# Optimization experiments

Hardware: AMD Instinct MI355X
Metric: run time of the kernel (lower is better)

The kernel has to match this reference:

```python
import jax, jax.numpy as jnp
import numpy as np

EPS_D = 1e-8   # clamp_min on knn distances
EPS_BN = 1e-5  # BatchNorm eps
K = 3


def _cdist(a, b):
    # a: (B,M,3), b: (B,N,3) -> (B,M,N) euclidean distances
    a2 = jnp.sum(a * a, axis=-1)[:, :, None]
    b2 = jnp.sum(b * b, axis=-1)[:, None, :]
    ab = jnp.einsum('bmd,bnd->bmn', a, b)
    return jnp.sqrt(jnp.maximum(a2 + b2 - 2.0 * ab, 0.0))


def _bn_relu(x, gamma, beta):
    # x: (B,C,N); BatchNorm1d training-mode math (biased batch stats) + ReLU
    mean = jnp.mean(x, axis=(0, 2), keepdims=True)
    var = jnp.mean((x - mean) ** 2, axis=(0, 2), keepdims=True)
    xn = (x - mean) * jax.lax.rsqrt(var + EPS_BN)
    return jax.nn.relu(xn * gamma[None, :, None] + beta[None, :, None])


def setup_inputs() -> dict:
    key = jax.random.key(0)
    ks = jax.random.split(key, 6)
    B, N1, N2, C1, C2 = 8, 8192, 2048, 128, 256
    xyz1 = jax.random.normal(ks[0], (B, N1, 3), dtype=jnp.float32)
    xyz2 = jax.random.normal(ks[1], (B, N2, 3), dtype=jnp.float32)
    feats1 = jax.random.normal(ks[2], (B, C1, N1), dtype=jnp.float32)
    feats2 = jax.random.normal(ks[3], (B, C2, N2), dtype=jnp.float32)
    in_ch = C2 + C1  # 384
    W1 = jax.random.normal(ks[4], (256, in_ch), dtype=jnp.float32) * 0.05
    b1 = jnp.zeros((256,), jnp.float32)
    g1 = jnp.ones((256,), jnp.float32)
    be1 = jnp.zeros((256,), jnp.float32)
    W2 = jax.random.normal(ks[5], (128, 256), dtype=jnp.float32) * 0.05
    b2 = jnp.zeros((128,), jnp.float32)
    g2 = jnp.ones((128,), jnp.float32)
    be2 = jnp.zeros((128,), jnp.float32)
    return {"xyz1": xyz1, "xyz2": xyz2, "feats1": feats1, "feats2": feats2,
            "W1": W1, "b1": b1, "g1": g1, "be1": be1,
            "W2": W2, "b2": b2, "g2": g2, "be2": be2}


def reference(xyz1, xyz2, feats1, feats2, W1, b1, g1, be1, W2, b2, g2, be2):
    # --- KNN interpolation ---
    d = _cdist(xyz1, xyz2)                       # (B,N1,N2)
    _, idx = jax.lax.top_k(-d, K)                # smallest-K indices (B,N1,K)
    knn_d = jnp.take_along_axis(d, idx, axis=2)  # (B,N1,K)
    w = 1.0 / jnp.maximum(knn_d, EPS_D)
    w = w / jnp.sum(w, axis=-1, keepdims=True)
    f2p = jnp.swapaxes(feats2, 1, 2)             # (B,N2,C2)
    neigh = jax.vmap(lambda f, i: f[i])(f2p, idx)  # (B,N1,K,C2)
    out = jnp.einsum('bmk,bmkc->bmc', w, neigh)  # (B,N1,C2)
    out = jnp.swapaxes(out, 1, 2)                # (B,C2,N1)
    out = jnp.concatenate([out, feats1], axis=1) # (B,C2+C1,N1)
    # --- Conv1d(1)-BN-ReLU MLP ---
    h = jnp.einsum('oc,bcn->bon', W1, out) + b1[None, :, None]
    h = _bn_relu(h, g1, be1)
    h = jnp.einsum('oc,bcn->bon', W2, h) + b2[None, :, None]
    h = _bn_relu(h, g2, be2)
    return h
```

## Files before the change

kernel.cpp:

```cpp
#include <hip/hip_runtime.h>

typedef __attribute__((ext_vector_type(8))) short short8;
typedef __attribute__((ext_vector_type(4))) float f32x4;

#define GLDS(gp, lp) __builtin_amdgcn_global_load_lds( \
    (const __attribute__((address_space(1))) void*)(gp), \
    (__attribute__((address_space(3))) void*)(lp), 16, 0, 0)

__device__ __forceinline__ unsigned short f2bf(float f){
    unsigned u = __float_as_uint(f);
    unsigned r = (u + 0x7fffu + ((u >> 16) & 1u)) >> 16;
    return (unsigned short)r;
}
__device__ __forceinline__ float bf2f(unsigned short s){
    return __uint_as_float(((unsigned)s) << 16);
}

__global__ __launch_bounds__(256) void cast_w_kernel(const float* __restrict__ W1, const float* __restrict__ W2,
                                                     unsigned short* __restrict__ W1c, unsigned short* __restrict__ W2c){
    int i = blockIdx.x * 256 + threadIdx.x;
    if (i < 98304) W1c[i] = f2bf(W1[i]);
    if (i < 32768) W2c[i] = f2bf(W2[i]);
}

__global__ void zero_stats_kernel(float* __restrict__ s){
    int i = blockIdx.x * 256 + threadIdx.x;
    if (i < 768) s[i] = 0.f;
}

__global__ __launch_bounds__(256) void knn_kernel(const float* __restrict__ xyz1, const float* __restrict__ xyz2,
                                                  int* __restrict__ oi, float* __restrict__ ow){
    __shared__ float sx[2048], sy[2048], sz[2048];
    __shared__ float sd[64][25];
    __shared__ int   si[64][25];
    int blk = blockIdx.x;
    int b  = blk >> 7;
    int n0 = (blk & 127) << 6;
    const float* p2 = xyz2 + (size_t)b * 2048 * 3;
    for (int j = threadIdx.x; j < 2048; j += 256){
        sx[j] = p2[j*3+0]; sy[j] = p2[j*3+1]; sz[j] = p2[j*3+2];
    }
    __syncthreads();
    int pp = threadIdx.x & 31, sub = threadIdx.x >> 5;
    int pA = n0 + pp, pB = pA + 32;
    const float* qa = xyz1 + ((size_t)b * 8192 + pA) * 3;
    float ax = qa[0], ay = qa[1], az = qa[2];
    float bx = qa[96], by = qa[97], bz = qa[98];
    float A0 = 1e30f, A1 = 1e30f, A2 = 1e30f; int Ai0 = 0, Ai1 = 0, Ai2 = 0;
    float B0 = 1e30f, B1 = 1e30f, B2 = 1e30f; int Bi0 = 0, Bi1 = 0, Bi2 = 0;
    int jb = sub << 8;
#pragma unroll 2
    for (int i = 0; i < 256; i += 4){
        f32x4 cx = *(const f32x4*)&sx[jb + i];
        f32x4 cy = *(const f32x4*)&sy[jb + i];
        f32x4 cz = *(const f32x4*)&sz[jb + i];
#pragma unroll
        for (int u = 0; u < 4; ++u){
            int j = jb + i + u;
            float dxA = ax - cx[u], dyA = ay - cy[u], dzA = az - cz[u];
            float dA = fmaf(dxA, dxA, fmaf(dyA, dyA, dzA * dzA));
            float dxB = bx - cx[u], dyB = by - cy[u], dzB = bz - cz[u];
            float dB = fmaf(dxB, dxB, fmaf(dyB, dyB, dzB * dzB));
            if (dA < A2){
                if (dA < A1){
                    A2 = A1; Ai2 = Ai1;
                    if (dA < A0){ A1 = A0; Ai1 = Ai0; A0 = dA; Ai0 = j; }
                    else        { A1 = dA; Ai1 = j; }
                } else { A2 = dA; Ai2 = j; }
            }
            if (dB < B2){
                if (dB < B1){
                    B2 = B1; Bi2 = Bi1;
                    if (dB < B0){ B1 = B0; Bi1 = Bi0; B0 = dB; Bi0 = j; }
                    else        { B1 = dB; Bi1 = j; }
                } else { B2 = dB; Bi2 = j; }
            }
        }
    }
    int c = sub * 3;
    sd[pp][c] = A0; sd[pp][c+1] = A1; sd[pp][c+2] = A2;
    si[pp][c] = Ai0; si[pp][c+1] = Ai1; si[pp][c+2] = Ai2;
    sd[pp+32][c] = B0; sd[pp+32][c+1] = B1; sd[pp+32][c+2] = B2;
    si[pp+32][c] = Bi0; si[pp+32][c+1] = Bi1; si[pp+32][c+2] = Bi2;
    __syncthreads();
    if (threadIdx.x < 64){
        int lp = threadIdx.x;
        float d0 = 1e30f, d1 = 1e30f, d2 = 1e30f;
        int i0 = 0, i1 = 0, i2 = 0;
#pragma unroll
        for (int k = 0; k < 24; ++k){
            float d = sd[lp][k]; int j = si[lp][k];
            if (d < d2){
                if (d < d1){
                    d2 = d1; i2 = i1;
                    if (d < d0){ d1 = d0; i1 = i0; d0 = d; i0 = j; }
                    else        { d1 = d;  i1 = j; }
                } else { d2 = d; i2 = j; }
            }
        }
        float w0 = 1.f / fmaxf(sqrtf(d0), 1e-8f);
        float w1 = 1.f / fmaxf(sqrtf(d1), 1e-8f);
        float w2 = 1.f / fmaxf(sqrtf(d2), 1e-8f);
        float inv = 1.f / (w0 + w1 + w2);
        int n = n0 + lp;
        size_t pbase = ((size_t)b * 8192 + n) * 3;
        ow[pbase + 0] = w0 * inv; ow[pbase + 1] = w1 * inv; ow[pbase + 2] = w2 * inv;
        oi[pbase + 0] = i0;       oi[pbase + 1] = i1;       oi[pbase + 2] = i2;
    }
}

__global__ __launch_bounds__(256) void transpose_f2_kernel(const float* __restrict__ f2, unsigned short* __restrict__ f2t){
    __shared__ float tile[32][33];
    int b = blockIdx.z, c0 = blockIdx.y * 32, n0 = blockIdx.x * 32;
    int tx = threadIdx.x, ty = threadIdx.y;
    for (int i = 0; i < 32; i += 8)
        tile[ty + i][tx] = f2[((size_t)b * 256 + c0 + ty + i) * 2048 + n0 + tx];
    __syncthreads();
    for (int i = 0; i < 32; i += 8)
        f2t[((size_t)b * 2048 + n0 + ty + i) * 256 + c0 + tx] = f2bf(tile[tx][ty + i]);
}

__global__ __launch_bounds__(128) void interp_kernel(const int* __restrict__ ki, const float* __restrict__ kw,
                                                     const unsigned short* __restrict__ f2t, unsigned short* __restrict__ X){
    int p = blockIdx.x;
    int b = p >> 13;
    const int*   ip = ki + (size_t)p * 3;
    const float* wp = kw + (size_t)p * 3;
    int i0 = ip[0], i1 = ip[1], i2 = ip[2];
    float w0 = wp[0], w1 = wp[1], w2 = wp[2];
    int t = threadIdx.x;
    const unsigned* f0 = (const unsigned*)(f2t + ((size_t)b * 2048 + i0) * 256);
    const unsigned* f1 = (const unsigned*)(f2t + ((size_t)b * 2048 + i1) * 256);
    const unsigned* f2 = (const unsigned*)(f2t + ((size_t)b * 2048 + i2) * 256);
    unsigned a = f0[t], c = f1[t], d = f2[t];
    float r0 = w0 * bf2f((unsigned short)(a & 0xffff)) + w1 * bf2f((unsigned short)(c & 0xffff)) + w2 * bf2f((unsigned short)(d & 0xffff));
    float r1 = w0 * bf2f((unsigned short)(a >> 16))   + w1 * bf2f((unsigned short)(c >> 16))   + w2 * bf2f((unsigned short)(d >> 16));
    ((unsigned*)(X + (size_t)p * 384))[t] = (unsigned)f2bf(r0) | ((unsigned)f2bf(r1) << 16);
}

__global__ __launch_bounds__(256) void transpose_f1_kernel(const float* __restrict__ f1, unsigned short* __restrict__ X){
    __shared__ float tile[32][33];
    int b = blockIdx.z, c0 = blockIdx.y * 32, n0 = blockIdx.x * 32;
    int tx = threadIdx.x, ty = threadIdx.y;
    for (int i = 0; i < 32; i += 8)
        tile[ty + i][tx] = f1[((size_t)b * 128 + c0 + ty + i) * 8192 + n0 + tx];
    __syncthreads();
    for (int i = 0; i < 32; i += 8)
        X[((size_t)b * 8192 + n0 + ty + i) * 384 + 256 + c0 + tx] = f2bf(tile[tx][ty + i]);
}

template<int KT, bool OBF>
__global__ __launch_bounds__(256) void gemm_bt(const unsigned short* __restrict__ A, const unsigned short* __restrict__ Bt,
                                               const float* __restrict__ bias, void* __restrict__ Cout,
                                               float* __restrict__ gsum, float* __restrict__ gsq, int Ncols){
    __shared__ unsigned short As[128 * 32];
    __shared__ unsigned short Bs[128 * 32];
    __shared__ float sLs[128], sLq[128];
    int tid = threadIdx.x;
    if (tid < 128){ sLs[tid] = 0.f; sLq[tid] = 0.f; }
    int m0 = blockIdx.x * 128;
    int n0 = blockIdx.y * 128;
    int lane = tid & 63, wid = tid >> 6;
    int m_w = (wid >> 1) * 64, n_w = (wid & 1) * 64;
    f32x4 acc[4][4] = {};

    int srow = tid >> 2, schunk = tid & 3;
    const char* Ab = (const char*)A + ((size_t)(m0 + srow) * KT + schunk * 8) * 2;
    const char* Bb = (const char*)Bt + ((size_t)(n0 + srow) * KT + schunk * 8) * 2;
    char* Asl = (char*)As + tid * 16;
    char* Bsl = (char*)Bs + tid * 16;
    const size_t rstep = (size_t)64 * KT * 2;

    int lr = lane & 15, lq = lane >> 4;
    for (int kt = 0; kt < KT / 32; ++kt){
        size_t koff = (size_t)kt * 64;
        GLDS(Ab + koff, Asl);
        GLDS(Ab + koff + rstep, Asl + 4096);
        GLDS(Bb + koff, Bsl);
        GLDS(Bb + koff + rstep, Bsl + 4096);
        __syncthreads();
        short8 af[4], bfr[4];
#pragma unroll
        for (int mf = 0; mf < 4; ++mf)
            af[mf] = *(const short8*)(As + (m_w + mf * 16 + lr) * 32 + lq * 8);
#pragma unroll
        for (int nf = 0; nf < 4; ++nf)
            bfr[nf] = *(const short8*)(Bs + (n_w + nf * 16 + lr) * 32 + lq * 8);
#pragma unroll
        for (int mf = 0; mf < 4; ++mf)
#pragma unroll
            for (int nf = 0; nf < 4; ++nf)
                acc[mf][nf] = __builtin_amdgcn_mfma_f32_16x16x32_bf16(af[mf], bfr[nf], acc[mf][nf], 0, 0, 0);
        __syncthreads();
    }

#pragma unroll
    for (int nf = 0; nf < 4; ++nf){
        int cl = n_w + nf * 16 + lr;
        int gc = n0 + cl;
        float bv = bias[gc];
        float ps = 0.f, pq = 0.f;
#pragma unroll
        for (int mf = 0; mf < 4; ++mf){
            int grow = m0 + m_w + mf * 16 + lq * 4;
#pragma unroll
            for (int r = 0; r < 4; ++r){
                float v = acc[mf][nf][r] + bv;
                size_t off = (size_t)(grow + r) * Ncols + gc;
                if (OBF) ((unsigned short*)Cout)[off] = f2bf(v);
                else     ((float*)Cout)[off] = v;
                ps += v; pq += v * v;
            }
        }
        ps += __shfl_xor(ps, 16); ps += __shfl_xor(ps, 32);
        pq += __shfl_xor(pq, 16); pq += __shfl_xor(pq, 32);
        if (lq == 0){ atomicAdd(&sLs[cl], ps); atomicAdd(&sLq[cl], pq); }
    }
    __syncthreads();
    if (tid < 128){
        atomicAdd(&gsum[n0 + tid], sLs[tid]);
        atomicAdd(&gsq[n0 + tid],  sLq[tid]);
    }
}

__global__ __launch_bounds__(256) void bn_relu_bf16(unsigned short* __restrict__ h, const float* __restrict__ gsum,
                                                    const float* __restrict__ gsq, const float* __restrict__ gamma,
                                                    const float* __restrict__ beta){
    const float inv = 1.0f / 65536.0f;
    size_t total2 = (size_t)65536 * 128;
    unsigned* hp = (unsigned*)h;
    for (size_t i = (size_t)blockIdx.x * blockDim.x + threadIdx.x; i < total2; i += (size_t)gridDim.x * blockDim.x){
        int c0 = (int)((i * 2) & 255);
        unsigned v = hp[i];
        float x0 = bf2f((unsigned short)(v & 0xffff));
        float x1 = bf2f((unsigned short)(v >> 16));
        float m0 = gsum[c0] * inv,     m1 = gsum[c0 + 1] * inv;
        float va0 = gsq[c0] * inv - m0 * m0, va1 = gsq[c0 + 1] * inv - m1 * m1;
        float rs0 = rsqrtf(va0 + 1e-5f), rs1 = rsqrtf(va1 + 1e-5f);
        float y0 = fmaxf((x0 - m0) * rs0 * gamma[c0] + beta[c0], 0.f);
        float y1 = fmaxf((x1 - m1) * rs1 * gamma[c0 + 1] + beta[c0 + 1], 0.f);
        hp[i] = (unsigned)f2bf(y0) | ((unsigned)f2bf(y1) << 16);
    }
}

__global__ __launch_bounds__(256) void bn2_transpose_kernel(const float* __restrict__ h2, const float* __restrict__ gsum,
                                                            const float* __restrict__ gsq, const float* __restrict__ g2,
                                                            const float* __restrict__ be2, float* __restrict__ out){
    __shared__ float tile[32][33];
    const float inv = 1.0f / 65536.0f;
    int b = blockIdx.z, o0 = blockIdx.y * 32, n0 = blockIdx.x * 32;
    int tx = threadIdx.x, ty = threadIdx.y;
    for (int i = 0; i < 32; i += 8)
        tile[ty + i][tx] = h2[((size_t)b * 8192 + n0 + ty + i) * 128 + o0 + tx];
    __syncthreads();
    for (int i = 0; i < 32; i += 8){
        int ch = o0 + ty + i;
        float m = gsum[ch] * inv;
        float va = gsq[ch] * inv - m * m;
        float rs = rsqrtf(va + 1e-5f);
        float sc = g2[ch] * rs, sh = be2[ch] - m * sc;
        float v = fmaxf(tile[tx][ty + i] * sc + sh, 0.f);
        out[((size_t)b * 128 + ch) * 8192 + n0 + tx] = v;
    }
}

extern "C" void kernel_launch(void* const* d_in, const int* in_sizes, int n_in,
                              void* d_out, int out_size, void* d_ws, size_t ws_size,
                              hipStream_t stream){
    const float* xyz1   = (const float*)d_in[0];
    const float* xyz2   = (const float*)d_in[1];
    const float* feats1 = (const float*)d_in[2];
    const float* feats2 = (const float*)d_in[3];
    const float* W1  = (const float*)d_in[4];
    const float* b1  = (const float*)d_in[5];
    const float* g1  = (const float*)d_in[6];
    const float* be1 = (const float*)d_in[7];
    const float* W2  = (const float*)d_in[8];
    const float* b2  = (const float*)d_in[9];
    const float* g2  = (const float*)d_in[10];
    const float* be2 = (const float*)d_in[11];
    float* out = (float*)d_out;

    char* p = (char*)d_ws;
    auto take = [&](size_t bytes) -> char* {
        char* r = p; p += (bytes + 255) & ~(size_t)255; return r;
    };
    unsigned short* W1c = (unsigned short*)take((size_t)98304 * 2);
    unsigned short* W2c = (unsigned short*)take((size_t)32768 * 2);
    int*   ki    = (int*)take((size_t)65536 * 3 * 4);
    float* kw    = (float*)take((size_t)65536 * 3 * 4);
    float* stats = (float*)take(768 * 4);
    unsigned short* f2t = (unsigned short*)take((size_t)8 * 2048 * 256 * 2);
    unsigned short* X   = (unsigned short*)take((size_t)65536 * 384 * 2);
    unsigned short* h1  = (unsigned short*)take((size_t)65536 * 256 * 2);
    float* h2 = (float*)X;

    float* s1 = stats, *q1 = stats + 256, *s2 = stats + 512, *q2 = stats + 640;

    zero_stats_kernel<<<dim3(3), 256, 0, stream>>>(stats);
    cast_w_kernel<<<dim3(384), 256, 0, stream>>>(W1, W2, W1c, W2c);
    knn_kernel<<<dim3(1024), 256, 0, stream>>>(xyz1, xyz2, ki, kw);
    transpose_f2_kernel<<<dim3(64, 8, 8), dim3(32, 8), 0, stream>>>(feats2, f2t);
    interp_kernel<<<dim3(65536), 128, 0, stream>>>(ki, kw, f2t, X);
    transpose_f1_kernel<<<dim3(256, 4, 8), dim3(32, 8), 0, stream>>>(feats1, X);
    gemm_bt<384, true><<<dim3(512, 2), 256, 0, stream>>>(X, W1c, b1, h1, s1, q1, 256);
    bn_relu_bf16<<<dim3(2048), 256, 0, stream>>>(h1, s1, q1, g1, be1);
    gemm_bt<256, false><<<dim3(512, 1), 256, 0, stream>>>(h1, W2c, b2, h2, s2, q2, 128);
    bn2_transpose_kernel<<<dim3(256, 4, 8), dim3(32, 8), 0, stream>>>(h2, s2, q2, g2, be2, out);
}
```

Before: 300.7 us.

## Branchless top-3 insertion, vectorized interp gather, merge init kernels

Replaces the nested-branch top-3 insertion in the KNN kernel with predicated selects, aiming to avoid wave divergence in the hot loop. Rewrites the interpolation kernel so each 8-thread group handles one point with 16-byte loads and stores, cutting the grid from 65536 tiny blocks to 2048. Also merges the stats-zeroing kernel into the weight-cast kernel to save a launch. The select form always does the extra register moves, which can cost ALU work when insertions are rare.

```diff
diff --git a/kernel.cpp b/kernel.cpp
--- a/kernel.cpp
+++ b/kernel.cpp
@@ -16,16 +16,13 @@
     return __uint_as_float(((unsigned)s) << 16);
 }
 
-__global__ __launch_bounds__(256) void cast_w_kernel(const float* __restrict__ W1, const float* __restrict__ W2,
-                                                     unsigned short* __restrict__ W1c, unsigned short* __restrict__ W2c){
+__global__ __launch_bounds__(256) void init_kernel(const float* __restrict__ W1, const float* __restrict__ W2,
+                                                   unsigned short* __restrict__ W1c, unsigned short* __restrict__ W2c,
+                                                   float* __restrict__ stats){
     int i = blockIdx.x * 256 + threadIdx.x;
     if (i < 98304) W1c[i] = f2bf(W1[i]);
     if (i < 32768) W2c[i] = f2bf(W2[i]);
-}
-
-__global__ void zero_stats_kernel(float* __restrict__ s){
-    int i = blockIdx.x * 256 + threadIdx.x;
-    if (i < 768) s[i] = 0.f;
+    if (i < 768) stats[i] = 0.f;
 }
 
 __global__ __launch_bounds__(256) void knn_kernel(const float* __restrict__ xyz1, const float* __restrict__ xyz2,
@@ -42,7 +39,7 @@
     }
     __syncthreads();
     int pp = threadIdx.x & 31, sub = threadIdx.x >> 5;
-    int pA = n0 + pp, pB = pA + 32;
+    int pA = n0 + pp;
     const float* qa = xyz1 + ((size_t)b * 8192 + pA) * 3;
     float ax = qa[0], ay = qa[1], az = qa[2];
     float bx = qa[96], by = qa[97], bz = qa[98];
@@ -61,19 +58,23 @@
             float dA = fmaf(dxA, dxA, fmaf(dyA, dyA, dzA * dzA));
             float dxB = bx - cx[u], dyB = by - cy[u], dzB = bz - cz[u];
             float dB = fmaf(dxB, dxB, fmaf(dyB, dyB, dzB * dzB));
-            if (dA < A2){
-                if (dA < A1){
-                    A2 = A1; Ai2 = Ai1;
-                    if (dA < A0){ A1 = A0; Ai1 = Ai0; A0 = dA; Ai0 = j; }
-                    else        { A1 = dA; Ai1 = j; }
-                } else { A2 = dA; Ai2 = j; }
+            {
+                bool c2 = dA < A2, c1 = dA < A1, c0 = dA < A0;
+                A2  = c1 ? A1  : (c2 ? dA : A2);
+                Ai2 = c1 ? Ai1 : (c2 ? j  : Ai2);
+                A1  = c0 ? A0  : (c1 ? dA : A1);
+                Ai1 = c0 ? Ai0 : (c1 ? j  : Ai1);
+                A0  = c0 ? dA  : A0;
+                Ai0 = c0 ? j   : Ai0;
             }
-            if (dB < B2){
-                if (dB < B1){
-                    B2 = B1; Bi2 = Bi1;
-                    if (dB < B0){ B1 = B0; Bi1 = Bi0; B0 = dB; Bi0 = j; }
-                    else        { B1 = dB; Bi1 = j; }
-                } else { B2 = dB; Bi2 = j; }
+            {
+                bool c2 = dB < B2, c1 = dB < B1, c0 = dB < B0;
+                B2  = c1 ? B1  : (c2 ? dB : B2);
+                Bi2 = c1 ? Bi1 : (c2 ? j  : Bi2);
+                B1  = c0 ? B0  : (c1 ? dB : B1);
+                Bi1 = c0 ? Bi0 : (c1 ? j  : Bi1);
+                B0  = c0 ? dB  : B0;
+                Bi0 = c0 ? j   : Bi0;
             }
         }
     }
@@ -90,13 +91,13 @@
 #pragma unroll
         for (int k = 0; k < 24; ++k){
             float d = sd[lp][k]; int j = si[lp][k];
-            if (d < d2){
-                if (d < d1){
-                    d2 = d1; i2 = i1;
-                    if (d < d0){ d1 = d0; i1 = i0; d0 = d; i0 = j; }
-                    else        { d1 = d;  i1 = j; }
-                } else { d2 = d; i2 = j; }
-            }
+            bool c2 = d < d2, c1 = d < d1, c0 = d < d0;
+            d2 = c1 ? d1 : (c2 ? d : d2);
+            i2 = c1 ? i1 : (c2 ? j : i2);
+            d1 = c0 ? d0 : (c1 ? d : d1);
+            i1 = c0 ? i0 : (c1 ? j : i1);
+            d0 = c0 ? d  : d0;
+            i0 = c0 ? j  : i0;
         }
         float w0 = 1.f / fmaxf(sqrtf(d0), 1e-8f);
         float w1 = 1.f / fmaxf(sqrtf(d1), 1e-8f);
@@ -120,22 +121,39 @@
         f2t[((size_t)b * 2048 + n0 + ty + i) * 256 + c0 + tx] = f2bf(tile[tx][ty + i]);
 }
 
-__global__ __launch_bounds__(128) void interp_kernel(const int* __restrict__ ki, const float* __restrict__ kw,
+__global__ __launch_bounds__(256) void interp_kernel(const int* __restrict__ ki, const float* __restrict__ kw,
                                                      const unsigned short* __restrict__ f2t, unsigned short* __restrict__ X){
-    int p = blockIdx.x;
+    int t = threadIdx.x;
+    int p = blockIdx.x * 32 + (t >> 3);
+    int q = t & 7;
     int b = p >> 13;
     const int*   ip = ki + (size_t)p * 3;
     const float* wp = kw + (size_t)p * 3;
     int i0 = ip[0], i1 = ip[1], i2 = ip[2];
     float w0 = wp[0], w1 = wp[1], w2 = wp[2];
-    int t = threadIdx.x;
-    const unsigned* f0 = (const unsigned*)(f2t + ((size_t)b * 2048 + i0) * 256);
-    const unsigned* f1 = (const unsigned*)(f2t + ((size_t)b * 2048 + i1) * 256);
-    const unsigned* f2 = (const unsigned*)(f2t + ((size_t)b * 2048 + i2) * 256);
-    unsigned a = f0[t], c = f1[t], d = f2[t];
-    float r0 = w0 * bf2f((unsigned short)(a & 0xffff)) + w1 * bf2f((unsigned short)(c & 0xffff)) + w2 * bf2f((unsigned short)(d & 0xffff));
-    float r1 = w0 * bf2f((unsigned short)(a >> 16))   + w1 * bf2f((unsigned short)(c >> 16))   + w2 * bf2f((unsigned short)(d >> 16));
-    ((unsigned*)(X + (size_t)p * 384))[t] = (unsigned)f2bf(r0) | ((unsigned)f2bf(r1) << 16);
+    const uint4* F0 = (const uint4*)(f2t + ((size_t)b * 2048 + i0) * 256);
+    const uint4* F1 = (const uint4*)(f2t + ((size_t)b * 2048 + i1) * 256);
+    const uint4* F2 = (const uint4*)(f2t + ((size_t)b * 2048 + i2) * 256);
+    uint4* Xp = (uint4*)(X + (size_t)p * 384);
+#pragma unroll
+    for (int s = 0; s < 4; ++s){
+        int ch = q + s * 8;
+        uint4 a = F0[ch], c = F1[ch], d = F2[ch];
+        uint4 r;
+        unsigned* ap = (unsigned*)&a; unsigned* cp = (unsigned*)&c;
+        unsigned* dp = (unsigned*)&d; unsigned* rp = (unsigned*)&r;
+#pragma unroll
+        for (int u = 0; u < 4; ++u){
+            float lo = w0 * bf2f((unsigned short)(ap[u] & 0xffff))
+                     + w1 * bf2f((unsigned short)(cp[u] & 0xffff))
+                     + w2 * bf2f((unsigned short)(dp[u] & 0xffff));
+            float hi = w0 * bf2f((unsigned short)(ap[u] >> 16))
+                     + w1 * bf2f((unsigned short)(cp[u] >> 16))
+                     + w2 * bf2f((unsigned short)(dp[u] >> 16));
+            rp[u] = (unsigned)f2bf(lo) | ((unsigned)f2bf(hi) << 16);
+        }
+        Xp[ch] = r;
+    }
 }
 
 __global__ __launch_bounds__(256) void transpose_f1_kernel(const float* __restrict__ f1, unsigned short* __restrict__ X){
@@ -297,11 +315,10 @@
 
     float* s1 = stats, *q1 = stats + 256, *s2 = stats + 512, *q2 = stats + 640;
 
-    zero_stats_kernel<<<dim3(3), 256, 0, stream>>>(stats);
-    cast_w_kernel<<<dim3(384), 256, 0, stream>>>(W1, W2, W1c, W2c);
+    init_kernel<<<dim3(384), 256, 0, stream>>>(W1, W2, W1c, W2c, stats);
     knn_kernel<<<dim3(1024), 256, 0, stream>>>(xyz1, xyz2, ki, kw);
     transpose_f2_kernel<<<dim3(64, 8, 8), dim3(32, 8), 0, stream>>>(feats2, f2t);
-    interp_kernel<<<dim3(65536), 128, 0, stream>>>(ki, kw, f2t, X);
+    interp_kernel<<<dim3(2048), 256, 0, stream>>>(ki, kw, f2t, X);
     transpose_f1_kernel<<<dim3(256, 4, 8), dim3(32, 8), 0, stream>>>(feats1, X);
     gemm_bt<384, true><<<dim3(512, 2), 256, 0, stream>>>(X, W1c, b1, h1, s1, q1, 256);
     bn_relu_bf16<<<dim3(2048), 256, 0, stream>>>(h1, s1, q1, g1, be1);
```

Result: no change. 300.8 us (+0.0%).
